# Performance work log

Measured on AMD Instinct MI355X. Metric: run time of the kernel, lower is better.

The kernel has to match this reference:

```python
import jax, jax.numpy as jnp
import numpy as np

HIDDEN = 128
N_HEADS = 8
SEQ = 4096


def setup_inputs() -> dict:
    key = jax.random.key(0)
    ks = jax.random.split(key, 7)
    H, NH = HIDDEN, N_HEADS
    s = 1.0 / np.sqrt(H)
    return {
        "x": jax.random.normal(ks[0], (SEQ, H), dtype=jnp.float32),
        "W1": jax.random.uniform(ks[1], (H, H * NH), jnp.float32, -s, s),
        "b1": jax.random.uniform(ks[2], (H * NH,), jnp.float32, -s, s),
        "W2": jax.random.uniform(ks[3], (H, H * NH), jnp.float32, -s, s),
        "b2": jax.random.uniform(ks[4], (H * NH,), jnp.float32, -s, s),
        "Wc": jax.random.uniform(ks[5], (H * NH, H), jnp.float32, -1.0 / np.sqrt(H * NH), 1.0 / np.sqrt(H * NH)),
        "bc": jax.random.uniform(ks[6], (H,), jnp.float32, -1.0 / np.sqrt(H * NH), 1.0 / np.sqrt(H * NH)),
    }


def reference(x, W1, b1, W2, b2, Wc, bc):
    S, H = x.shape
    NH = W1.shape[1] // H
    # project then split into heads: [S, NH*H] -> [NH, S, H]
    q1 = (x @ W1 + b1).reshape(S, NH, H).transpose(1, 0, 2)
    q2 = (x @ W2 + b2).reshape(S, NH, H).transpose(1, 0, 2)
    # unscaled attention scores per head: [NH, S, S]
    att = jax.nn.softmax(jnp.einsum('hse,hte->hst', q1, q2), axis=-1)
    # weighted sum of q2 (values == q2 in this module): [NH, S, H]
    ctx = jnp.einsum('hst,hte->hse', att, q2)
    # concat heads back along feature dim: [S, NH*H]
    ctx = ctx.transpose(1, 0, 2).reshape(S, NH * H)
    return ctx @ Wc + bc + x
```

## Files before the change

kernel.cpp:

```cpp
#include <hip/hip_runtime.h>

#define H 128
#define NHEADS 8
#define SQ 4096
#define HD 1024

typedef float f32x4 __attribute__((ext_vector_type(4)));
typedef __bf16 bf16x8 __attribute__((ext_vector_type(8)));
typedef unsigned short u16x4 __attribute__((ext_vector_type(4)));
typedef unsigned short u16x8 __attribute__((ext_vector_type(8)));
typedef unsigned int u32x4 __attribute__((ext_vector_type(4)));

static __device__ __forceinline__ unsigned short f2bf(float f) {
  unsigned int u = __builtin_bit_cast(unsigned int, f);
  u += 0x7fffu + ((u >> 16) & 1u);
  return (unsigned short)(u >> 16);
}
static __device__ __forceinline__ float b2f(unsigned short s) {
  unsigned int u = (unsigned int)s << 16;
  return __builtin_bit_cast(float, u);
}
static __device__ __forceinline__ bf16x8 ld_bf8(const unsigned short* p) {
  return __builtin_bit_cast(bf16x8, *(const u16x8*)p);
}

__global__ __launch_bounds__(256) void prep_kernel(
    const float* __restrict__ W1, const float* __restrict__ W2,
    const float* __restrict__ Wc,
    unsigned short* __restrict__ W1T, unsigned short* __restrict__ W2T,
    unsigned short* __restrict__ WcT)
{
  __shared__ unsigned short tile[64 * 66];
  const int b = blockIdx.x, tid = threadIdx.x;
  if (b < 32) {
    const int k0 = (b & 1) * 64, n0 = (b >> 1) * 64;
    for (int i = 0; i < 16; ++i) {
      int idx = tid + i * 256;
      int r = idx >> 6, cc = idx & 63;
      tile[cc * 66 + r] = f2bf(W1[(size_t)(k0 + r) * HD + n0 + cc]);
    }
    __syncthreads();
    for (int i = 0; i < 16; ++i) {
      int idx = tid + i * 256;
      int r = idx >> 6, cc = idx & 63;
      W1T[(size_t)(n0 + r) * H + k0 + cc] = tile[r * 66 + cc];
    }
    __syncthreads();
    for (int i = 0; i < 16; ++i) {
      int idx = tid + i * 256;
      int r = idx >> 6, cc = idx & 63;
      tile[cc * 66 + r] = f2bf(W2[(size_t)(k0 + r) * HD + n0 + cc]);
    }
    __syncthreads();
    for (int i = 0; i < 16; ++i) {
      int idx = tid + i * 256;
      int r = idx >> 6, cc = idx & 63;
      W2T[(size_t)(n0 + r) * H + k0 + cc] = tile[r * 66 + cc];
    }
  } else {
    const int bb = b - 32;
    const int n0 = (bb & 1) * 64, k0 = (bb >> 1) * 64;
    for (int i = 0; i < 16; ++i) {
      int idx = tid + i * 256;
      int r = idx >> 6, cc = idx & 63;
      tile[cc * 66 + r] = f2bf(Wc[(size_t)(k0 + r) * H + n0 + cc]);
    }
    __syncthreads();
    for (int i = 0; i < 16; ++i) {
      int idx = tid + i * 256;
      int r = idx >> 6, cc = idx & 63;
      WcT[(size_t)(n0 + r) * HD + k0 + cc] = tile[r * 66 + cc];
    }
  }
}

__global__ __launch_bounds__(256) void proj_kernel(
    const float* __restrict__ x,
    const float* __restrict__ b1, const float* __restrict__ b2,
    const unsigned short* __restrict__ W1T, const unsigned short* __restrict__ W2T,
    unsigned short* __restrict__ q1bf, unsigned short* __restrict__ q2K,
    unsigned short* __restrict__ q2VT)
{
  __shared__ unsigned short At[64 * 136];
  __shared__ unsigned short Bt[128 * 136];
  const int tid = threadIdx.x;
  const int st = blockIdx.x & 63, h = blockIdx.x >> 6;
  const int s0 = st * 64;
  const int lane = tid & 63, w = tid >> 6;
  const int c = lane & 15, q4 = lane >> 4;

  for (int i = 0; i < 4; ++i) {
    int ch = tid + i * 256;
    int row = ch >> 4, col8 = (ch & 15) * 8;
    const float* gp = x + (s0 + row) * H + col8;
    f32x4 a = *(const f32x4*)gp;
    f32x4 b = *(const f32x4*)(gp + 4);
    u16x8 v;
    v[0]=f2bf(a[0]); v[1]=f2bf(a[1]); v[2]=f2bf(a[2]); v[3]=f2bf(a[3]);
    v[4]=f2bf(b[0]); v[5]=f2bf(b[1]); v[6]=f2bf(b[2]); v[7]=f2bf(b[3]);
    *(u16x8*)&At[row * 136 + col8] = v;
  }
  for (int i = 0; i < 8; ++i) {
    int ch = tid + i * 256;
    int row = ch >> 4, col8 = (ch & 15) * 8;
    *(u16x8*)&Bt[row * 136 + col8] = *(const u16x8*)&W1T[(h * H + row) * H + col8];
  }
  __syncthreads();

  bf16x8 af[4];
  for (int kc = 0; kc < 4; ++kc)
    af[kc] = ld_bf8(&At[(w * 16 + c) * 136 + kc * 32 + q4 * 8]);
  __syncthreads();

  for (int nt = 0; nt < 8; ++nt) {
    f32x4 acc = {0.f, 0.f, 0.f, 0.f};
    for (int kc = 0; kc < 4; ++kc) {
      bf16x8 bf = ld_bf8(&Bt[(nt * 16 + c) * 136 + kc * 32 + q4 * 8]);
      acc = __builtin_amdgcn_mfma_f32_16x16x32_bf16(af[kc], bf, acc, 0, 0, 0);
    }
    float bb = b1[h * H + nt * 16 + c];
    for (int r = 0; r < 4; ++r)
      At[(w * 16 + q4 * 4 + r) * 136 + nt * 16 + c] = f2bf(acc[r] + bb);
  }
  __syncthreads();

  for (int i = 0; i < 4; ++i) {
    int ch = tid + i * 256;
    int row = ch >> 4, col8 = (ch & 15) * 8;
    *(u16x8*)&q1bf[(size_t)(h * SQ + s0 + row) * H + col8] =
        *(const u16x8*)&At[row * 136 + col8];
  }
  for (int i = 0; i < 8; ++i) {
    int ch = tid + i * 256;
    int row = ch >> 4, col8 = (ch & 15) * 8;
    *(u16x8*)&Bt[row * 136 + col8] = *(const u16x8*)&W2T[(h * H + row) * H + col8];
  }
  __syncthreads();

  f32x4 q2a[8];
  for (int nt = 0; nt < 8; ++nt) {
    f32x4 acc = {0.f, 0.f, 0.f, 0.f};
    for (int kc = 0; kc < 4; ++kc) {
      bf16x8 bf = ld_bf8(&Bt[(nt * 16 + c) * 136 + kc * 32 + q4 * 8]);
      acc = __builtin_amdgcn_mfma_f32_16x16x32_bf16(af[kc], bf, acc, 0, 0, 0);
    }
    q2a[nt] = acc;
  }
  __syncthreads();

  for (int nt = 0; nt < 8; ++nt) {
    float bb = b2[h * H + nt * 16 + c];
    unsigned short vs[4];
    for (int r = 0; r < 4; ++r) {
      unsigned short u = f2bf(q2a[nt][r] + bb);
      At[(w * 16 + q4 * 4 + r) * 136 + nt * 16 + c] = u;
      vs[r] = u;
    }
    u16x4 v4 = {vs[0], vs[1], vs[2], vs[3]};
    *(u16x4*)&Bt[(nt * 16 + c) * 72 + w * 16 + q4 * 4] = v4;
  }
  __syncthreads();

  for (int i = 0; i < 4; ++i) {
    int ch = tid + i * 256;
    int row = ch >> 4, col8 = (ch & 15) * 8;
    *(u16x8*)&q2K[(size_t)(h * SQ + s0 + row) * H + col8] =
        *(const u16x8*)&At[row * 136 + col8];
  }
  for (int i = 0; i < 4; ++i) {
    int ch = tid + i * 256;
    int row = ch >> 3, col8 = (ch & 7) * 8;
    *(u16x8*)&q2VT[(size_t)(h * H + row) * SQ + s0 + col8] =
        *(const u16x8*)&Bt[row * 72 + col8];
  }
}

__global__ __launch_bounds__(256, 2) void flash_kernel(
    const unsigned short* __restrict__ q1bf,
    const unsigned short* __restrict__ q2K,
    const unsigned short* __restrict__ q2VT,
    unsigned short* __restrict__ ctxp,
    float* __restrict__ lbuf)
{
  __shared__ unsigned short Kt[64 * 128];
  __shared__ unsigned short VT[128 * 64];
  const int tid = threadIdx.x;
  const int bid = blockIdx.x;
  const int kb = bid >> 8;
  const int h = (bid >> 5) & 7, qb = bid & 31;
  const int s0 = qb * 128;
  const int kbase = kb * 2048;
  const int lane = tid & 63, w = tid >> 6;
  const int c = lane & 15, q4 = lane >> 4;

  bf16x8 qf[2][4];
  for (int blk = 0; blk < 2; ++blk)
    for (int kc = 0; kc < 4; ++kc)
      qf[blk][kc] = ld_bf8(
          &q1bf[(h * SQ + s0 + w * 32 + blk * 16 + c) * H + kc * 32 + q4 * 8]);

  f32x4 acc[2][8];
  for (int blk = 0; blk < 2; ++blk)
    for (int nt = 0; nt < 8; ++nt) acc[blk][nt] = (f32x4){0.f, 0.f, 0.f, 0.f};
  float lsum[2] = {0.f, 0.f};

  u16x8 kreg[4], vreg[4];
  for (int i = 0; i < 4; ++i) {
    int ch = tid + i * 256;
    kreg[i] = *(const u16x8*)&q2K[(h * SQ + kbase + (ch >> 4)) * H + (ch & 15) * 8];
    vreg[i] = *(const u16x8*)&q2VT[(h * H + (ch >> 3)) * SQ + kbase + (ch & 7) * 8];
  }

  for (int kt = 0; kt < 32; ++kt) {
    if (kt) __syncthreads();
    for (int i = 0; i < 4; ++i) {
      int ch = tid + i * 256;
      {
        int row = ch >> 4, chunk = (ch & 15) ^ (row & 7);
        *(u16x8*)&Kt[row * 128 + chunk * 8] = kreg[i];
      }
      {
        int row = ch >> 3, chunk = (ch & 7) ^ (row & 7);
        *(u16x8*)&VT[row * 64 + chunk * 8] = vreg[i];
      }
    }
    __syncthreads();

    if (kt < 31) {
      const int k0 = kbase + (kt + 1) * 64;
      for (int i = 0; i < 4; ++i) {
        int ch = tid + i * 256;
        kreg[i] = *(const u16x8*)&q2K[(h * SQ + k0 + (ch >> 4)) * H + (ch & 15) * 8];
        vreg[i] = *(const u16x8*)&q2VT[(h * H + (ch >> 3)) * SQ + k0 + (ch & 7) * 8];
      }
    }

    f32x4 sc[2][4];
    for (int mt = 0; mt < 4; ++mt) {
      bf16x8 kf[4];
      for (int kc = 0; kc < 4; ++kc) {
        int chunk = (kc * 4 + q4) ^ (c & 7);
        kf[kc] = ld_bf8(&Kt[(mt * 16 + c) * 128 + chunk * 8]);
      }
      for (int blk = 0; blk < 2; ++blk) {
        f32x4 s = {0.f, 0.f, 0.f, 0.f};
        for (int kc = 0; kc < 4; ++kc)
          s = __builtin_amdgcn_mfma_f32_16x16x32_bf16(kf[kc], qf[blk][kc], s, 0, 0, 0);
        sc[blk][mt] = s;
      }
    }

    unsigned int pw[2][4][2];
#pragma unroll
    for (int blk = 0; blk < 2; ++blk) {
      float ts = 0.f;
#pragma unroll
      for (int mt = 0; mt < 4; ++mt) {
        f32x4 p;
        for (int r = 0; r < 4; ++r) { p[r] = __expf(sc[blk][mt][r]); ts += p[r]; }
        sc[blk][mt] = p;
      }
      lsum[blk] += ts;
#pragma unroll
      for (int mt = 0; mt < 4; ++mt) {
        pw[blk][mt][0] = (unsigned int)f2bf(sc[blk][mt][0]) |
                         ((unsigned int)f2bf(sc[blk][mt][1]) << 16);
        pw[blk][mt][1] = (unsigned int)f2bf(sc[blk][mt][2]) |
                         ((unsigned int)f2bf(sc[blk][mt][3]) << 16);
      }
    }

#pragma unroll
    for (int kc2 = 0; kc2 < 2; ++kc2) {
      u32x4 pa = {pw[0][2 * kc2][0], pw[0][2 * kc2][1],
                  pw[0][2 * kc2 + 1][0], pw[0][2 * kc2 + 1][1]};
      u32x4 pb = {pw[1][2 * kc2][0], pw[1][2 * kc2][1],
                  pw[1][2 * kc2 + 1][0], pw[1][2 * kc2 + 1][1]};
      bf16x8 pf0 = __builtin_bit_cast(bf16x8, pa);
      bf16x8 pf1 = __builtin_bit_cast(bf16x8, pb);
      const int clo = (4 * kc2 + (q4 >> 1)) ^ (c & 7);
      const int chi = (4 * kc2 + 2 + (q4 >> 1)) ^ (c & 7);
      const int sub = (q4 & 1) * 4;
      for (int nt = 0; nt < 8; ++nt) {
        const unsigned short* vrow = &VT[(nt * 16 + c) * 64];
        u16x4 vlo = *(const u16x4*)(vrow + clo * 8 + sub);
        u16x4 vhi = *(const u16x4*)(vrow + chi * 8 + sub);
        bf16x8 vf = __builtin_bit_cast(bf16x8,
            __builtin_shufflevector(vlo, vhi, 0, 1, 2, 3, 4, 5, 6, 7));
        acc[0][nt] = __builtin_amdgcn_mfma_f32_16x16x32_bf16(pf0, vf, acc[0][nt], 0, 0, 0);
        acc[1][nt] = __builtin_amdgcn_mfma_f32_16x16x32_bf16(pf1, vf, acc[1][nt], 0, 0, 0);
      }
    }
  }

  unsigned short* ctxk = ctxp + (size_t)kb * SQ * HD;
  for (int blk = 0; blk < 2; ++blk) {
    float l = lsum[blk];
    l += __shfl_xor(l, 16);
    l += __shfl_xor(l, 32);
    float rl = 1.f / l;
    if (q4 == 0)
      lbuf[(size_t)kb * NHEADS * SQ + h * SQ + s0 + w * 32 + blk * 16 + c] = l;
    float r0 = __shfl(rl, q4 * 4 + 0);
    float r1 = __shfl(rl, q4 * 4 + 1);
    float r2 = __shfl(rl, q4 * 4 + 2);
    float r3 = __shfl(rl, q4 * 4 + 3);
    for (int nt = 0; nt < 8; ++nt) {
      int col = h * H + nt * 16 + c;
      int srow = s0 + w * 32 + blk * 16 + q4 * 4;
      ctxk[(size_t)(srow + 0) * HD + col] = f2bf(acc[blk][nt][0] * r0);
      ctxk[(size_t)(srow + 1) * HD + col] = f2bf(acc[blk][nt][1] * r1);
      ctxk[(size_t)(srow + 2) * HD + col] = f2bf(acc[blk][nt][2] * r2);
      ctxk[(size_t)(srow + 3) * HD + col] = f2bf(acc[blk][nt][3] * r3);
    }
  }
}

__global__ __launch_bounds__(256) void out_kernel(
    const unsigned short* __restrict__ ctxp,
    const float* __restrict__ lbuf,
    const unsigned short* __restrict__ WcT,
    const float* __restrict__ bc,
    const float* __restrict__ x,
    float* __restrict__ out)
{
  __shared__ unsigned short At[16 * 136];
  __shared__ unsigned short Bt[128 * 136];
  const int tid = threadIdx.x;
  const int s0 = blockIdx.x * 16;
  const int lane = tid & 63, w = tid >> 6;
  const int c = lane & 15, q4 = lane >> 4;

  f32x4 acc[2];
  acc[0] = (f32x4){0.f, 0.f, 0.f, 0.f};
  acc[1] = (f32x4){0.f, 0.f, 0.f, 0.f};

  for (int kt = 0; kt < 8; ++kt) {
    __syncthreads();
    {
      int row = tid >> 4, col8 = (tid & 15) * 8;
      const unsigned short* p0 = &ctxp[(size_t)(s0 + row) * HD + kt * 128 + col8];
      u16x8 a0 = *(const u16x8*)p0;
      u16x8 a1 = *(const u16x8*)(p0 + (size_t)SQ * HD);
      float la = lbuf[(size_t)kt * SQ + s0 + row];
      float lb = lbuf[(size_t)NHEADS * SQ + (size_t)kt * SQ + s0 + row];
      float ri = 1.f / (la + lb);
      float wa = la * ri, wb = lb * ri;
      u16x8 av;
      for (int e = 0; e < 8; ++e)
        av[e] = f2bf(wa * b2f(a0[e]) + wb * b2f(a1[e]));
      *(u16x8*)&At[row * 136 + col8] = av;
    }
    for (int i = 0; i < 8; ++i) {
      int ch = tid + i * 256;
      int row = ch >> 4, col8 = (ch & 15) * 8;
      *(u16x8*)&Bt[row * 136 + col8] =
          *(const u16x8*)&WcT[row * HD + kt * 128 + col8];
    }
    __syncthreads();
    bf16x8 af[4];
    for (int kc = 0; kc < 4; ++kc)
      af[kc] = ld_bf8(&At[c * 136 + kc * 32 + q4 * 8]);
    for (int j = 0; j < 2; ++j) {
      int nt = w * 2 + j;
      f32x4 a = acc[j];
      for (int kc = 0; kc < 4; ++kc) {
        bf16x8 bf = ld_bf8(&Bt[(nt * 16 + c) * 136 + kc * 32 + q4 * 8]);
        a = __builtin_amdgcn_mfma_f32_16x16x32_bf16(af[kc], bf, a, 0, 0, 0);
      }
      acc[j] = a;
    }
  }
  for (int j = 0; j < 2; ++j) {
    int nt = w * 2 + j;
    float bb = bc[nt * 16 + c];
    for (int r = 0; r < 4; ++r) {
      int srow = s0 + q4 * 4 + r;
      int col = nt * 16 + c;
      out[srow * H + col] = acc[j][r] + bb + x[srow * H + col];
    }
  }
}

extern "C" void kernel_launch(void* const* d_in, const int* in_sizes, int n_in,
                              void* d_out, int out_size, void* d_ws, size_t ws_size,
                              hipStream_t stream) {
  const float* x  = (const float*)d_in[0];
  const float* W1 = (const float*)d_in[1];
  const float* b1 = (const float*)d_in[2];
  const float* W2 = (const float*)d_in[3];
  const float* b2 = (const float*)d_in[4];
  const float* Wc = (const float*)d_in[5];
  const float* bc = (const float*)d_in[6];
  float* out = (float*)d_out;

  char* ws = (char*)d_ws;
  unsigned short* q1bf = (unsigned short*)ws; ws += (size_t)NHEADS * SQ * H * 2;
  unsigned short* q2K  = (unsigned short*)ws; ws += (size_t)NHEADS * SQ * H * 2;
  unsigned short* q2VT = (unsigned short*)ws; ws += (size_t)NHEADS * SQ * H * 2;
  unsigned short* ctxp = (unsigned short*)ws; ws += (size_t)2 * SQ * HD * 2;
  float*          lbuf = (float*)ws;          ws += (size_t)2 * NHEADS * SQ * 4;
  unsigned short* W1T  = (unsigned short*)ws; ws += (size_t)HD * H * 2;
  unsigned short* W2T  = (unsigned short*)ws; ws += (size_t)HD * H * 2;
  unsigned short* WcT  = (unsigned short*)ws; ws += (size_t)HD * H * 2;

  prep_kernel<<<64, 256, 0, stream>>>(W1, W2, Wc, W1T, W2T, WcT);
  proj_kernel<<<512, 256, 0, stream>>>(x, b1, b2, W1T, W2T, q1bf, q2K, q2VT);
  flash_kernel<<<512, 256, 0, stream>>>(q1bf, q2K, q2VT, ctxp, lbuf);
  out_kernel<<<256, 256, 0, stream>>>(ctxp, lbuf, WcT, bc, x, out);
}
```

Measured before the change: 179.7 us.

## Stream K/V tiles directly into double-buffered LDS with global_load_lds

The flash kernel no longer stages K and V^T tiles through registers and then copies them into shared memory. Each thread now issues 16-byte global-to-LDS DMA loads into a second LDS buffer while the current buffer is being consumed. The XOR swizzle moves from the LDS write address to the global read address, since the LDS destination is fixed per wave. This frees the staging registers and removes one barrier per iteration, at the cost of doubling LDS use per block to 64 KB. It also relies on the compiler waiting for the asynchronous loads to finish before the barrier.

```diff
diff --git a/kernel.cpp b/kernel.cpp
--- a/kernel.cpp
+++ b/kernel.cpp
@@ -23,6 +23,11 @@
 static __device__ __forceinline__ bf16x8 ld_bf8(const unsigned short* p) {
   return __builtin_bit_cast(bf16x8, *(const u16x8*)p);
 }
+
+#define GLOAD_LDS16(gp, lp)                                        \
+  __builtin_amdgcn_global_load_lds(                                \
+      (__attribute__((address_space(1))) void*)(gp),               \
+      (__attribute__((address_space(3))) void*)(lp), 16, 0, 0)
 
 __global__ __launch_bounds__(256) void prep_kernel(
     const float* __restrict__ W1, const float* __restrict__ W2,
@@ -182,8 +187,8 @@
     unsigned short* __restrict__ ctxp,
     float* __restrict__ lbuf)
 {
-  __shared__ unsigned short Kt[64 * 128];
-  __shared__ unsigned short VT[128 * 64];
+  __shared__ unsigned short Kt[2][64 * 128];
+  __shared__ unsigned short VT[2][128 * 64];
   const int tid = threadIdx.x;
   const int bid = blockIdx.x;
   const int kb = bid >> 8;
@@ -192,6 +197,7 @@
   const int kbase = kb * 2048;
   const int lane = tid & 63, w = tid >> 6;
   const int c = lane & 15, q4 = lane >> 4;
+  const int wch = tid & 192;
 
   bf16x8 qf[2][4];
   for (int blk = 0; blk < 2; ++blk)
@@ -204,43 +210,36 @@
     for (int nt = 0; nt < 8; ++nt) acc[blk][nt] = (f32x4){0.f, 0.f, 0.f, 0.f};
   float lsum[2] = {0.f, 0.f};
 
-  u16x8 kreg[4], vreg[4];
-  for (int i = 0; i < 4; ++i) {
-    int ch = tid + i * 256;
-    kreg[i] = *(const u16x8*)&q2K[(h * SQ + kbase + (ch >> 4)) * H + (ch & 15) * 8];
-    vreg[i] = *(const u16x8*)&q2VT[(h * H + (ch >> 3)) * SQ + kbase + (ch & 7) * 8];
-  }
-
-  for (int kt = 0; kt < 32; ++kt) {
-    if (kt) __syncthreads();
+  auto stage = [&](int buf, int k0) {
+#pragma unroll
     for (int i = 0; i < 4; ++i) {
       int ch = tid + i * 256;
-      {
-        int row = ch >> 4, chunk = (ch & 15) ^ (row & 7);
-        *(u16x8*)&Kt[row * 128 + chunk * 8] = kreg[i];
-      }
-      {
-        int row = ch >> 3, chunk = (ch & 7) ^ (row & 7);
-        *(u16x8*)&VT[row * 64 + chunk * 8] = vreg[i];
-      }
-    }
-    __syncthreads();
-
-    if (kt < 31) {
-      const int k0 = kbase + (kt + 1) * 64;
-      for (int i = 0; i < 4; ++i) {
-        int ch = tid + i * 256;
-        kreg[i] = *(const u16x8*)&q2K[(h * SQ + k0 + (ch >> 4)) * H + (ch & 15) * 8];
-        vreg[i] = *(const u16x8*)&q2VT[(h * H + (ch >> 3)) * SQ + k0 + (ch & 7) * 8];
-      }
-    }
+      int krow = ch >> 4;
+      int kchunk = (ch & 15) ^ (krow & 7);
+      GLOAD_LDS16(q2K + (size_t)(h * SQ + k0 + krow) * H + kchunk * 8,
+                  &Kt[buf][(i * 256 + wch) * 8]);
+      int vrow = ch >> 3;
+      int vchunk = (ch & 7) ^ (vrow & 7);
+      GLOAD_LDS16(q2VT + (size_t)(h * H + vrow) * SQ + k0 + vchunk * 8,
+                  &VT[buf][(i * 256 + wch) * 8]);
+    }
+  };
+
+  stage(0, kbase);
+
+  for (int kt = 0; kt < 32; ++kt) {
+    const int cur = kt & 1;
+    __syncthreads();
+
+    if (kt < 31)
+      stage(cur ^ 1, kbase + (kt + 1) * 64);
 
     f32x4 sc[2][4];
     for (int mt = 0; mt < 4; ++mt) {
       bf16x8 kf[4];
       for (int kc = 0; kc < 4; ++kc) {
         int chunk = (kc * 4 + q4) ^ (c & 7);
-        kf[kc] = ld_bf8(&Kt[(mt * 16 + c) * 128 + chunk * 8]);
+        kf[kc] = ld_bf8(&Kt[cur][(mt * 16 + c) * 128 + chunk * 8]);
       }
       for (int blk = 0; blk < 2; ++blk) {
         f32x4 s = {0.f, 0.f, 0.f, 0.f};
@@ -282,7 +281,7 @@
       const int chi = (4 * kc2 + 2 + (q4 >> 1)) ^ (c & 7);
       const int sub = (q4 & 1) * 4;
       for (int nt = 0; nt < 8; ++nt) {
-        const unsigned short* vrow = &VT[(nt * 16 + c) * 64];
+        const unsigned short* vrow = &VT[cur][(nt * 16 + c) * 64];
         u16x4 vlo = *(const u16x4*)(vrow + clo * 8 + sub);
         u16x4 vhi = *(const u16x4*)(vrow + chi * 8 + sub);
         bf16x8 vf = __builtin_bit_cast(bf16x8,
```

After: 179.8 us. No clear change (+0.0%).
